# Kernel optimization log

Measured on AMD Instinct MI355X. Metric: run time of the kernel, lower is better.

## Reference

```python
import jax, jax.numpy as jnp
import numpy as np

B, N, D, H = 32, 128, 64, 128


def setup_inputs() -> dict:
    key = jax.random.key(0)
    ks = jax.random.split(key, 16)
    s = 0.05
    inp = {
        "x": jax.random.normal(ks[0], (B, N, D), dtype=jnp.float32),
        "masks": jax.random.randint(ks[1], (B, N), 0, 2, dtype=jnp.int32),
        # message_net: Linear(2D,H) -> ReLU -> Linear(H,H)
        "W1": jax.random.normal(ks[2], (2 * D, H), dtype=jnp.float32) * s,
        "b1": jax.random.normal(ks[3], (H,), dtype=jnp.float32) * s,
        "W2": jax.random.normal(ks[4], (H, H), dtype=jnp.float32) * s,
        "b2": jax.random.normal(ks[5], (H,), dtype=jnp.float32) * s,
        # attention_net: Linear(2D,H) -> ReLU -> Linear(H,1)
        "A1": jax.random.normal(ks[6], (2 * D, H), dtype=jnp.float32) * s,
        "ab1": jax.random.normal(ks[7], (H,), dtype=jnp.float32) * s,
        "A2": jax.random.normal(ks[8], (H, 1), dtype=jnp.float32) * s,
        "ab2": jax.random.normal(ks[9], (1,), dtype=jnp.float32) * s,
        # update_net: Linear(D+H,H) -> ReLU -> Linear(H,D)
        "U1": jax.random.normal(ks[10], (D + H, H), dtype=jnp.float32) * s,
        "ub1": jax.random.normal(ks[11], (H,), dtype=jnp.float32) * s,
        "U2": jax.random.normal(ks[12], (H, D), dtype=jnp.float32) * s,
        "ub2": jax.random.normal(ks[13], (D,), dtype=jnp.float32) * s,
    }
    return inp


def reference(x, masks, W1, b1, W2, b2, A1, ab1, A2, ab2, U1, ub1, U2, ub2):
    d = x.shape[-1]
    # pairs = cat([x_i, x_j]); Linear(pairs) == x_i @ W[:d] + x_j @ W[d:] + b
    # message MLP hidden: (B, N, N, H)
    h = jax.nn.relu(
        jnp.einsum("bid,dh->bih", x, W1[:d])[:, :, None, :]
        + jnp.einsum("bjd,dh->bjh", x, W1[d:])[:, None, :, :]
        + b1
    )
    messages = jnp.einsum("bijh,hk->bijk", h, W2) + b2  # (B, N, N, H)
    # attention MLP
    ha = jax.nn.relu(
        jnp.einsum("bid,dh->bih", x, A1[:d])[:, :, None, :]
        + jnp.einsum("bjd,dh->bjh", x, A1[d:])[:, None, :, :]
        + ab1
    )
    logits = jnp.einsum("bijh,h->bij", ha, A2[:, 0]) + ab2[0]  # (B, N, N)
    m = masks.astype(bool)[:, None, :]  # mask over j (source agents)
    logits = jnp.where(m, logits, -jnp.inf)
    attn = jax.nn.softmax(logits, axis=-1)
    attn = jnp.where(m, attn, 0.0)
    agg = jnp.einsum("bijh,bij->bih", messages, attn)  # (B, N, H)
    comb = jnp.concatenate([x, agg], axis=-1)  # (B, N, D+H)
    upd = jax.nn.relu(comb @ U1 + ub1) @ U2 + ub2  # (B, N, D)
    return x + upd
```

## Files before the change

kernel.cpp:

```cpp
#include <hip/hip_runtime.h>
#include <hip/hip_bf16.h>
#include <stdint.h>

#define NN 128
#define DD 64
#define HH 128

__device__ __forceinline__ float bflo(uint32_t u){ union{uint32_t u;float f;} c; c.u = u<<16; return c.f; }
__device__ __forceinline__ float bfhi(uint32_t u){ union{uint32_t u;float f;} c; c.u = u & 0xffff0000u; return c.f; }
__device__ __forceinline__ uint32_t packbf(float lo, float hi){
  __hip_bfloat16 a = __float2bfloat16(lo);
  __hip_bfloat16 b = __float2bfloat16(hi);
  uint16_t ua = *(uint16_t*)&a, ub = *(uint16_t*)&b;
  return (uint32_t)ua | ((uint32_t)ub<<16);
}

__global__ __launch_bounds__(128) void k1_proj(
    const float* __restrict__ x,
    const float* __restrict__ W1, const float* __restrict__ b1,
    const float* __restrict__ A1, const float* __restrict__ ab1,
    const float* __restrict__ W2, const float* __restrict__ b2,
    const float* __restrict__ U1, const float* __restrict__ ub1,
    float* __restrict__ Pm, float* __restrict__ Pa,
    uint32_t* __restrict__ Qmp, uint32_t* __restrict__ Qap,
    float* __restrict__ M, float* __restrict__ c0){
  const int bid = blockIdx.x;
  const int t = threadIdx.x;
  if(bid >= 512){
    int hb = bid - 512;
    if(hb < HH){
      float acc = 0.f;
      #pragma unroll 4
      for(int k=0;k<HH;k++) acc += W2[hb*HH+k] * U1[(DD+k)*HH+t];
      M[hb*HH+t] = acc;
    } else {
      float acc = ub1[t];
      #pragma unroll 4
      for(int k=0;k<HH;k++) acc += b2[k] * U1[(DD+k)*HH+t];
      c0[t] = acc;
    }
    return;
  }
  const int g = bid & 15, b = bid >> 4;
  const int jb = g*4;
  __shared__ float xs[8][64];
  __shared__ float qmS[8][128];
  __shared__ float qaS[8][128];
  {
    int r = t >> 4, d4 = (t & 15)*4;
    int gr = (r<4) ? (jb+r) : (jb + r - 4 + 64);
    *(float4*)&xs[r][d4] = *(const float4*)&x[(b*NN+gr)*DD + d4];
  }
  __syncthreads();
  float pm[8], qm[8], pa[8], qa[8];
  #pragma unroll
  for(int r=0;r<8;r++){ pm[r]=0.f;qm[r]=0.f;pa[r]=0.f;qa[r]=0.f; }
  for(int d0=0; d0<DD; d0+=4){
    float4 xr[8];
    #pragma unroll
    for(int r=0;r<8;r++) xr[r] = *(const float4*)&xs[r][d0];
    #pragma unroll
    for(int dd=0; dd<4; dd++){
      const int d = d0 + dd;
      float w1a = W1[d*HH + t];
      float w1b = W1[(DD+d)*HH + t];
      float a1a = A1[d*HH + t];
      float a1b = A1[(DD+d)*HH + t];
      #pragma unroll
      for(int r=0;r<8;r++){
        float xv = (&xr[r].x)[dd];
        pm[r] += xv*w1a; qm[r] += xv*w1b;
        pa[r] += xv*a1a; qa[r] += xv*a1b;
      }
    }
  }
  float b1v = b1[t], ab1v = ab1[t];
  #pragma unroll
  for(int r=0;r<8;r++){
    int gr = (r<4) ? (jb+r) : (jb + r - 4 + 64);
    Pm[(b*NN+gr)*HH + t] = pm[r] + b1v;
    Pa[(b*NN+gr)*HH + t] = pa[r] + ab1v;
    qmS[r][t] = qm[r];
    qaS[r][t] = qa[r];
  }
  __syncthreads();
  #pragma unroll
  for(int k=0;k<4;k++){
    int idx = t + k*128;
    int r = idx >> 6, hp = idx & 63;
    int gr = (r<4) ? (jb+r) : (jb + r - 4 + 64);
    Qmp[(b*NN+gr)*64 + hp] = packbf(qmS[r][hp], qmS[r][hp+64]);
    Qap[(b*NN+gr)*64 + hp] = packbf(qaS[r][hp], qaS[r][hp+64]);
  }
}

__global__ __launch_bounds__(256) void k2_attn_hbar(
    const float* __restrict__ Pa, const float* __restrict__ Pm,
    const uint32_t* __restrict__ Qap, const uint32_t* __restrict__ Qmp,
    const float* __restrict__ A2, const int* __restrict__ masks,
    float* __restrict__ hbar){
  const int it = blockIdx.x;
  const int b  = blockIdx.y;
  const int t = threadIdx.x;
  const int wave = t>>6, lane = t&63;
  __shared__ uint32_t qbuf[NN*65];
  __shared__ float pS[8*HH];
  __shared__ float a2S[HH];
  __shared__ float atS[8*NN];
  {
    const uint32_t* src = Qap + (size_t)b*NN*64;
    #pragma unroll
    for(int k=0;k<8;k++){
      int idx4 = t + k*256;
      int j = idx4 >> 4, hp4 = (idx4 & 15)*4;
      uint4 v = *(const uint4*)&src[j*64 + hp4];
      uint32_t* d = &qbuf[j*65 + hp4];
      d[0]=v.x; d[1]=v.y; d[2]=v.z; d[3]=v.w;
    }
    int r = t>>5, h4 = (t&31)*4;
    *(float4*)&pS[r*HH + h4] = *(const float4*)&Pa[(b*NN + it*8 + r)*HH + h4];
    if(t < HH) a2S[t] = A2[t];
  }
  __syncthreads();
  const int i0 = wave*2, i1 = i0+1;
  float a00=0.f,a01=0.f,a10=0.f,a11=0.f;
  for(int h0=0; h0<64; h0+=4){
    float4 p0a = *(const float4*)&pS[i0*HH + h0];
    float4 p0b = *(const float4*)&pS[i0*HH + 64 + h0];
    float4 p1a = *(const float4*)&pS[i1*HH + h0];
    float4 p1b = *(const float4*)&pS[i1*HH + 64 + h0];
    float4 a2a = *(const float4*)&a2S[h0];
    float4 a2b = *(const float4*)&a2S[64 + h0];
    #pragma unroll
    for(int dd=0; dd<4; dd++){
      uint32_t q0 = qbuf[lane*65 + h0 + dd];
      uint32_t q1 = qbuf[(lane+64)*65 + h0 + dd];
      float q0l=bflo(q0), q0h=bfhi(q0), q1l=bflo(q1), q1h=bfhi(q1);
      float pa0=(&p0a.x)[dd], pb0=(&p0b.x)[dd];
      float pa1=(&p1a.x)[dd], pb1=(&p1b.x)[dd];
      float aa=(&a2a.x)[dd],  ab=(&a2b.x)[dd];
      a00 += fmaxf(pa0+q0l,0.f)*aa; a00 += fmaxf(pb0+q0h,0.f)*ab;
      a01 += fmaxf(pa0+q1l,0.f)*aa; a01 += fmaxf(pb0+q1h,0.f)*ab;
      a10 += fmaxf(pa1+q0l,0.f)*aa; a10 += fmaxf(pb1+q0h,0.f)*ab;
      a11 += fmaxf(pa1+q1l,0.f)*aa; a11 += fmaxf(pb1+q1h,0.f)*ab;
    }
  }
  const int m0 = masks[b*NN + lane];
  const int m1 = masks[b*NN + 64 + lane];
  const float NEG = -3.0e38f;
  #pragma unroll
  for(int ii=0; ii<2; ii++){
    float x0 = ii ? a10 : a00, x1 = ii ? a11 : a01;
    int il = ii ? i1 : i0;
    float l0 = m0 ? x0 : NEG, l1 = m1 ? x1 : NEG;
    float v = fmaxf(l0, l1);
    for(int off=32; off>=1; off>>=1) v = fmaxf(v, __shfl_xor(v, off));
    float e0 = m0 ? __expf(x0 - v) : 0.f;
    float e1 = m1 ? __expf(x1 - v) : 0.f;
    float s = e0 + e1;
    for(int off=32; off>=1; off>>=1) s += __shfl_xor(s, off);
    float inv = (s > 0.f) ? (1.f/s) : 0.f;
    atS[il*NN + lane]      = e0*inv;
    atS[il*NN + 64 + lane] = e1*inv;
  }
  __syncthreads();
  {
    const uint32_t* src = Qmp + (size_t)b*NN*64;
    #pragma unroll
    for(int k=0;k<8;k++){
      int idx4 = t + k*256;
      int j = idx4 >> 4, hp4 = (idx4 & 15)*4;
      uint4 v = *(const uint4*)&src[j*64 + hp4];
      uint32_t* d = &qbuf[j*65 + hp4];
      d[0]=v.x; d[1]=v.y; d[2]=v.z; d[3]=v.w;
    }
    int r = t>>5, h4 = (t&31)*4;
    *(float4*)&pS[r*HH + h4] = *(const float4*)&Pm[(b*NN + it*8 + r)*HH + h4];
  }
  __syncthreads();
  float pm00 = pS[i0*HH + lane], pm01 = pS[i0*HH + 64 + lane];
  float pm10 = pS[i1*HH + lane], pm11 = pS[i1*HH + 64 + lane];
  float h00=0.f,h01=0.f,h10=0.f,h11=0.f;
  for(int j0=0; j0<NN; j0+=4){
    float4 at0 = *(const float4*)&atS[i0*NN + j0];
    float4 at1 = *(const float4*)&atS[i1*NN + j0];
    #pragma unroll
    for(int dd=0; dd<4; dd++){
      uint32_t qd = qbuf[(j0+dd)*65 + lane];
      float ql = bflo(qd), qh = bfhi(qd);
      float w0 = (&at0.x)[dd], w1 = (&at1.x)[dd];
      h00 += w0*fmaxf(pm00+ql,0.f);
      h01 += w0*fmaxf(pm01+qh,0.f);
      h10 += w1*fmaxf(pm10+ql,0.f);
      h11 += w1*fmaxf(pm11+qh,0.f);
    }
  }
  const int gi0 = b*NN + it*8 + i0, gi1 = gi0 + 1;
  hbar[gi0*HH + lane]      = h00;
  hbar[gi0*HH + 64 + lane] = h01;
  hbar[gi1*HH + lane]      = h10;
  hbar[gi1*HH + 64 + lane] = h11;
}

__global__ __launch_bounds__(256) void k3_update(
    const float* __restrict__ x, const float* __restrict__ hbar,
    const float* __restrict__ M, const float* __restrict__ c0,
    const float* __restrict__ U1, const float* __restrict__ U2,
    const float* __restrict__ ub2, float* __restrict__ out){
  const int bid = blockIdx.x;
  const int t = threadIdx.x;
  const int r0 = bid*16;
  __shared__ float xs[16][64];
  __shared__ float hb[16][128];
  __shared__ float hidS[16][128];
  __shared__ float c0S[128];
  {
    int r = t>>4, d4 = (t&15)*4;
    *(float4*)&xs[r][d4] = *(const float4*)&x[(r0+r)*DD + d4];
    int r1 = t>>5, h4 = (t&31)*4;
    *(float4*)&hb[r1][h4]   = *(const float4*)&hbar[(r0+r1)*HH + h4];
    *(float4*)&hb[r1+8][h4] = *(const float4*)&hbar[(r0+r1+8)*HH + h4];
    if(t<128) c0S[t] = c0[t];
  }
  __syncthreads();
  {
    const int c = t & 127, g = t>>7;
    float acc[8];
    #pragma unroll
    for(int r=0;r<8;r++) acc[r]=0.f;
    for(int d0=0; d0<DD; d0+=4){
      float4 xr[8];
      #pragma unroll
      for(int r=0;r<8;r++) xr[r] = *(const float4*)&xs[g*8+r][d0];
      #pragma unroll
      for(int dd=0; dd<4; dd++){
        float u = U1[(d0+dd)*HH + c];
        #pragma unroll
        for(int r=0;r<8;r++) acc[r] += (&xr[r].x)[dd]*u;
      }
    }
    for(int h0=0; h0<HH; h0+=4){
      float4 hr[8];
      #pragma unroll
      for(int r=0;r<8;r++) hr[r] = *(const float4*)&hb[g*8+r][h0];
      #pragma unroll
      for(int dd=0; dd<4; dd++){
        float mv = M[(h0+dd)*HH + c];
        #pragma unroll
        for(int r=0;r<8;r++) acc[r] += (&hr[r].x)[dd]*mv;
      }
    }
    float cc = c0S[c];
    #pragma unroll
    for(int r=0;r<8;r++) hidS[g*8+r][c] = fmaxf(acc[r]+cc, 0.f);
  }
  __syncthreads();
  {
    const int dcol = t & 63, rg = t>>6;
    float acc2[4];
    #pragma unroll
    for(int r=0;r<4;r++) acc2[r]=0.f;
    for(int ci=0; ci<HH; ci+=4){
      float4 hr[4];
      #pragma unroll
      for(int r=0;r<4;r++) hr[r] = *(const float4*)&hidS[rg*4+r][ci];
      #pragma unroll
      for(int dd=0; dd<4; dd++){
        float u2 = U2[(ci+dd)*DD + dcol];
        #pragma unroll
        for(int r=0;r<4;r++) acc2[r] += (&hr[r].x)[dd]*u2;
      }
    }
    float ub = ub2[dcol];
    #pragma unroll
    for(int r=0;r<4;r++){
      int row = r0 + rg*4 + r;
      out[row*DD + dcol] = xs[rg*4+r][dcol] + acc2[r] + ub;
    }
  }
}

extern "C" void kernel_launch(void* const* d_in, const int* in_sizes, int n_in,
                              void* d_out, int out_size, void* d_ws, size_t ws_size,
                              hipStream_t stream){
  const float* x   = (const float*)d_in[0];
  const int*   msk = (const int*)d_in[1];
  const float* W1  = (const float*)d_in[2];
  const float* b1  = (const float*)d_in[3];
  const float* W2  = (const float*)d_in[4];
  const float* b2  = (const float*)d_in[5];
  const float* A1  = (const float*)d_in[6];
  const float* ab1 = (const float*)d_in[7];
  const float* A2  = (const float*)d_in[8];
  const float* U1  = (const float*)d_in[10];
  const float* ub1 = (const float*)d_in[11];
  const float* U2  = (const float*)d_in[12];
  const float* ub2 = (const float*)d_in[13];
  float* out = (float*)d_out;

  char* w = (char*)d_ws;
  float*    Pm   = (float*)(w);
  float*    Pa   = (float*)(w + (2u<<20));
  uint32_t* Qmp  = (uint32_t*)(w + (4u<<20));
  uint32_t* Qap  = (uint32_t*)(w + (5u<<20));
  float*    hbar = (float*)(w + (6u<<20));
  float*    M    = (float*)(w + (8u<<20));
  float*    c0   = (float*)(w + (8u<<20) + (64u<<10));

  hipLaunchKernelGGL(k1_proj, dim3(641), dim3(128), 0, stream,
                     x, W1, b1, A1, ab1, W2, b2, U1, ub1,
                     Pm, Pa, Qmp, Qap, M, c0);
  hipLaunchKernelGGL(k2_attn_hbar, dim3(16,32), dim3(256), 0, stream,
                     Pa, Pm, Qap, Qmp, A2, msk, hbar);
  hipLaunchKernelGGL(k3_update, dim3(256), dim3(256), 0, stream,
                     x, hbar, M, c0, U1, U2, ub2, out);
}
```

Before: 125.0 us.

## Fuse update MLP into attention kernel and vectorize LDS access

Merges the update MLP (k3) into the attention/aggregation kernel, so hbar stays in shared memory and one launch plus a global round trip go away. The attention logit loop now reads the bf16 Q buffer with 16-byte vector loads, using a padded stride of 68 and an interleaved layout for P and A2. The update matmuls use float4 reads of U1 and M per thread. In exchange, each 8-row block redoes the U1/M/U2 weight reads, and shared memory use per block grows, which may lower occupancy.

```diff
diff --git a/kernel.cpp b/kernel.cpp
--- a/kernel.cpp
+++ b/kernel.cpp
@@ -5,6 +5,7 @@
 #define NN 128
 #define DD 64
 #define HH 128
+#define QPAD 68
 
 __device__ __forceinline__ float bflo(uint32_t u){ union{uint32_t u;float f;} c; c.u = u<<16; return c.f; }
 __device__ __forceinline__ float bfhi(uint32_t u){ union{uint32_t u;float f;} c; c.u = u & 0xffff0000u; return c.f; }
@@ -13,6 +14,17 @@
   __hip_bfloat16 b = __float2bfloat16(hi);
   uint16_t ua = *(uint16_t*)&a, ub = *(uint16_t*)&b;
   return (uint32_t)ua | ((uint32_t)ub<<16);
+}
+
+__device__ __forceinline__ void acc4(uint32_t qd0, uint32_t qd1,
+                                     float2 p0, float2 p1, float2 a2,
+                                     float2& A00, float2& A01, float2& A10, float2& A11){
+  float2 q0 = make_float2(bflo(qd0), bfhi(qd0));
+  float2 q1 = make_float2(bflo(qd1), bfhi(qd1));
+  A00.x += fmaxf(p0.x+q0.x,0.f)*a2.x; A00.y += fmaxf(p0.y+q0.y,0.f)*a2.y;
+  A01.x += fmaxf(p0.x+q1.x,0.f)*a2.x; A01.y += fmaxf(p0.y+q1.y,0.f)*a2.y;
+  A10.x += fmaxf(p1.x+q0.x,0.f)*a2.x; A10.y += fmaxf(p1.y+q0.y,0.f)*a2.y;
+  A11.x += fmaxf(p1.x+q1.x,0.f)*a2.x; A11.y += fmaxf(p1.y+q1.y,0.f)*a2.y;
 }
 
 __global__ __launch_bounds__(128) void k1_proj(
@@ -94,74 +106,86 @@
   }
 }
 
-__global__ __launch_bounds__(256) void k2_attn_hbar(
+__global__ __launch_bounds__(256) void k2_fused(
     const float* __restrict__ Pa, const float* __restrict__ Pm,
     const uint32_t* __restrict__ Qap, const uint32_t* __restrict__ Qmp,
     const float* __restrict__ A2, const int* __restrict__ masks,
-    float* __restrict__ hbar){
+    const float* __restrict__ M, const float* __restrict__ c0,
+    const float* __restrict__ U1, const float* __restrict__ U2,
+    const float* __restrict__ ub2, const float* __restrict__ x,
+    float* __restrict__ out){
   const int it = blockIdx.x;
   const int b  = blockIdx.y;
   const int t = threadIdx.x;
   const int wave = t>>6, lane = t&63;
-  __shared__ uint32_t qbuf[NN*65];
-  __shared__ float pS[8*HH];
-  __shared__ float a2S[HH];
+  __shared__ uint32_t qbuf[NN*QPAD];
+  __shared__ float pSi[8*HH];
+  __shared__ float a2i[HH];
   __shared__ float atS[8*NN];
+  __shared__ float hbS[8*HH];
+  __shared__ float hidS[8*HH];
+  __shared__ float xs[8][64];
+  __shared__ float c0S[HH];
+  const int i0 = wave*2, i1 = i0+1;
+  const int row0 = b*NN + it*8;
   {
     const uint32_t* src = Qap + (size_t)b*NN*64;
     #pragma unroll
     for(int k=0;k<8;k++){
       int idx4 = t + k*256;
       int j = idx4 >> 4, hp4 = (idx4 & 15)*4;
-      uint4 v = *(const uint4*)&src[j*64 + hp4];
-      uint32_t* d = &qbuf[j*65 + hp4];
-      d[0]=v.x; d[1]=v.y; d[2]=v.z; d[3]=v.w;
-    }
-    int r = t>>5, h4 = (t&31)*4;
-    *(float4*)&pS[r*HH + h4] = *(const float4*)&Pa[(b*NN + it*8 + r)*HH + h4];
-    if(t < HH) a2S[t] = A2[t];
-  }
-  __syncthreads();
-  const int i0 = wave*2, i1 = i0+1;
-  float a00=0.f,a01=0.f,a10=0.f,a11=0.f;
-  for(int h0=0; h0<64; h0+=4){
-    float4 p0a = *(const float4*)&pS[i0*HH + h0];
-    float4 p0b = *(const float4*)&pS[i0*HH + 64 + h0];
-    float4 p1a = *(const float4*)&pS[i1*HH + h0];
-    float4 p1b = *(const float4*)&pS[i1*HH + 64 + h0];
-    float4 a2a = *(const float4*)&a2S[h0];
-    float4 a2b = *(const float4*)&a2S[64 + h0];
-    #pragma unroll
-    for(int dd=0; dd<4; dd++){
-      uint32_t q0 = qbuf[lane*65 + h0 + dd];
-      uint32_t q1 = qbuf[(lane+64)*65 + h0 + dd];
-      float q0l=bflo(q0), q0h=bfhi(q0), q1l=bflo(q1), q1h=bfhi(q1);
-      float pa0=(&p0a.x)[dd], pb0=(&p0b.x)[dd];
-      float pa1=(&p1a.x)[dd], pb1=(&p1b.x)[dd];
-      float aa=(&a2a.x)[dd],  ab=(&a2b.x)[dd];
-      a00 += fmaxf(pa0+q0l,0.f)*aa; a00 += fmaxf(pb0+q0h,0.f)*ab;
-      a01 += fmaxf(pa0+q1l,0.f)*aa; a01 += fmaxf(pb0+q1h,0.f)*ab;
-      a10 += fmaxf(pa1+q0l,0.f)*aa; a10 += fmaxf(pb1+q0h,0.f)*ab;
-      a11 += fmaxf(pa1+q1l,0.f)*aa; a11 += fmaxf(pb1+q1h,0.f)*ab;
-    }
+      *(uint4*)&qbuf[j*QPAD + hp4] = *(const uint4*)&src[j*64 + hp4];
+    }
+    #pragma unroll
+    for(int k=0;k<4;k++){
+      int idx = t + k*256;
+      int r = idx>>7, rem = idx&127, h2 = rem&63, half = rem>>6;
+      pSi[r*HH + 2*h2 + half] = Pa[(row0 + r)*HH + h2 + 64*half];
+    }
+    if(t < HH) a2i[2*(t&63) + (t>>6)] = A2[t];
+    if(t < 128){ int r = t>>4, d4 = (t&15)*4;
+      *(float4*)&xs[r][d4] = *(const float4*)&x[(row0 + r)*DD + d4]; }
+    else { int u = t-128; if(u < HH) c0S[u] = c0[u]; }
   }
   const int m0 = masks[b*NN + lane];
   const int m1 = masks[b*NN + 64 + lane];
-  const float NEG = -3.0e38f;
-  #pragma unroll
-  for(int ii=0; ii<2; ii++){
-    float x0 = ii ? a10 : a00, x1 = ii ? a11 : a01;
-    int il = ii ? i1 : i0;
-    float l0 = m0 ? x0 : NEG, l1 = m1 ? x1 : NEG;
-    float v = fmaxf(l0, l1);
-    for(int off=32; off>=1; off>>=1) v = fmaxf(v, __shfl_xor(v, off));
-    float e0 = m0 ? __expf(x0 - v) : 0.f;
-    float e1 = m1 ? __expf(x1 - v) : 0.f;
-    float s = e0 + e1;
-    for(int off=32; off>=1; off>>=1) s += __shfl_xor(s, off);
-    float inv = (s > 0.f) ? (1.f/s) : 0.f;
-    atS[il*NN + lane]      = e0*inv;
-    atS[il*NN + 64 + lane] = e1*inv;
+  __syncthreads();
+  {
+    float2 A00=make_float2(0.f,0.f), A01=A00, A10=A00, A11=A00;
+    for(int hp0=0; hp0<64; hp0+=4){
+      uint4 q0 = *(const uint4*)&qbuf[lane*QPAD + hp0];
+      uint4 q1 = *(const uint4*)&qbuf[(lane+64)*QPAD + hp0];
+      float4 p0a = *(const float4*)&pSi[i0*HH + 2*hp0];
+      float4 p0b = *(const float4*)&pSi[i0*HH + 2*hp0 + 4];
+      float4 p1a = *(const float4*)&pSi[i1*HH + 2*hp0];
+      float4 p1b = *(const float4*)&pSi[i1*HH + 2*hp0 + 4];
+      float4 aa  = *(const float4*)&a2i[2*hp0];
+      float4 ab  = *(const float4*)&a2i[2*hp0 + 4];
+      acc4(q0.x, q1.x, make_float2(p0a.x,p0a.y), make_float2(p1a.x,p1a.y),
+           make_float2(aa.x,aa.y), A00,A01,A10,A11);
+      acc4(q0.y, q1.y, make_float2(p0a.z,p0a.w), make_float2(p1a.z,p1a.w),
+           make_float2(aa.z,aa.w), A00,A01,A10,A11);
+      acc4(q0.z, q1.z, make_float2(p0b.x,p0b.y), make_float2(p1b.x,p1b.y),
+           make_float2(ab.x,ab.y), A00,A01,A10,A11);
+      acc4(q0.w, q1.w, make_float2(p0b.z,p0b.w), make_float2(p1b.z,p1b.w),
+           make_float2(ab.z,ab.w), A00,A01,A10,A11);
+    }
+    float l[2][2] = {{A00.x+A00.y, A01.x+A01.y},{A10.x+A10.y, A11.x+A11.y}};
+    const float NEG = -3.0e38f;
+    #pragma unroll
+    for(int ii=0; ii<2; ii++){
+      float x0 = l[ii][0], x1 = l[ii][1];
+      int il = i0 + ii;
+      float v = fmaxf(m0 ? x0 : NEG, m1 ? x1 : NEG);
+      for(int off=32; off>=1; off>>=1) v = fmaxf(v, __shfl_xor(v, off));
+      float e0 = m0 ? __expf(x0 - v) : 0.f;
+      float e1 = m1 ? __expf(x1 - v) : 0.f;
+      float s = e0 + e1;
+      for(int off=32; off>=1; off>>=1) s += __shfl_xor(s, off);
+      float inv = (s > 0.f) ? (1.f/s) : 0.f;
+      atS[il*NN + lane]      = e0*inv;
+      atS[il*NN + 64 + lane] = e1*inv;
+    }
   }
   __syncthreads();
   {
@@ -170,113 +194,81 @@
     for(int k=0;k<8;k++){
       int idx4 = t + k*256;
       int j = idx4 >> 4, hp4 = (idx4 & 15)*4;
-      uint4 v = *(const uint4*)&src[j*64 + hp4];
-      uint32_t* d = &qbuf[j*65 + hp4];
-      d[0]=v.x; d[1]=v.y; d[2]=v.z; d[3]=v.w;
-    }
-    int r = t>>5, h4 = (t&31)*4;
-    *(float4*)&pS[r*HH + h4] = *(const float4*)&Pm[(b*NN + it*8 + r)*HH + h4];
-  }
-  __syncthreads();
-  float pm00 = pS[i0*HH + lane], pm01 = pS[i0*HH + 64 + lane];
-  float pm10 = pS[i1*HH + lane], pm11 = pS[i1*HH + 64 + lane];
-  float h00=0.f,h01=0.f,h10=0.f,h11=0.f;
-  for(int j0=0; j0<NN; j0+=4){
-    float4 at0 = *(const float4*)&atS[i0*NN + j0];
-    float4 at1 = *(const float4*)&atS[i1*NN + j0];
-    #pragma unroll
-    for(int dd=0; dd<4; dd++){
-      uint32_t qd = qbuf[(j0+dd)*65 + lane];
-      float ql = bflo(qd), qh = bfhi(qd);
-      float w0 = (&at0.x)[dd], w1 = (&at1.x)[dd];
-      h00 += w0*fmaxf(pm00+ql,0.f);
-      h01 += w0*fmaxf(pm01+qh,0.f);
-      h10 += w1*fmaxf(pm10+ql,0.f);
-      h11 += w1*fmaxf(pm11+qh,0.f);
-    }
-  }
-  const int gi0 = b*NN + it*8 + i0, gi1 = gi0 + 1;
-  hbar[gi0*HH + lane]      = h00;
-  hbar[gi0*HH + 64 + lane] = h01;
-  hbar[gi1*HH + lane]      = h10;
-  hbar[gi1*HH + 64 + lane] = h11;
-}
-
-__global__ __launch_bounds__(256) void k3_update(
-    const float* __restrict__ x, const float* __restrict__ hbar,
-    const float* __restrict__ M, const float* __restrict__ c0,
-    const float* __restrict__ U1, const float* __restrict__ U2,
-    const float* __restrict__ ub2, float* __restrict__ out){
-  const int bid = blockIdx.x;
-  const int t = threadIdx.x;
-  const int r0 = bid*16;
-  __shared__ float xs[16][64];
-  __shared__ float hb[16][128];
-  __shared__ float hidS[16][128];
-  __shared__ float c0S[128];
-  {
-    int r = t>>4, d4 = (t&15)*4;
-    *(float4*)&xs[r][d4] = *(const float4*)&x[(r0+r)*DD + d4];
-    int r1 = t>>5, h4 = (t&31)*4;
-    *(float4*)&hb[r1][h4]   = *(const float4*)&hbar[(r0+r1)*HH + h4];
-    *(float4*)&hb[r1+8][h4] = *(const float4*)&hbar[(r0+r1+8)*HH + h4];
-    if(t<128) c0S[t] = c0[t];
-  }
-  __syncthreads();
-  {
-    const int c = t & 127, g = t>>7;
-    float acc[8];
-    #pragma unroll
-    for(int r=0;r<8;r++) acc[r]=0.f;
+      *(uint4*)&qbuf[j*QPAD + hp4] = *(const uint4*)&src[j*64 + hp4];
+    }
+    #pragma unroll
+    for(int k=0;k<4;k++){
+      int idx = t + k*256;
+      int r = idx>>7, rem = idx&127, h2 = rem&63, half = rem>>6;
+      pSi[r*HH + 2*h2 + half] = Pm[(row0 + r)*HH + h2 + 64*half];
+    }
+  }
+  __syncthreads();
+  {
+    float2 pm0 = *(const float2*)&pSi[i0*HH + 2*lane];
+    float2 pm1 = *(const float2*)&pSi[i1*HH + 2*lane];
+    float2 H0 = make_float2(0.f,0.f), H1 = H0;
+    for(int j0=0; j0<NN; j0+=4){
+      float4 at0 = *(const float4*)&atS[i0*NN + j0];
+      float4 at1 = *(const float4*)&atS[i1*NN + j0];
+      #pragma unroll
+      for(int dd=0; dd<4; dd++){
+        uint32_t qd = qbuf[(j0+dd)*QPAD + lane];
+        float ql = bflo(qd), qh = bfhi(qd);
+        float w0 = (&at0.x)[dd], w1 = (&at1.x)[dd];
+        H0.x += w0*fmaxf(pm0.x+ql,0.f); H0.y += w0*fmaxf(pm0.y+qh,0.f);
+        H1.x += w1*fmaxf(pm1.x+ql,0.f); H1.y += w1*fmaxf(pm1.y+qh,0.f);
+      }
+    }
+    hbS[i0*HH + lane]      = H0.x;
+    hbS[i0*HH + 64 + lane] = H0.y;
+    hbS[i1*HH + lane]      = H1.x;
+    hbS[i1*HH + 64 + lane] = H1.y;
+  }
+  __syncthreads();
+  {
+    const int r = t>>5, c4 = (t&31)*4;
+    float4 acc = *(const float4*)&c0S[c4];
     for(int d0=0; d0<DD; d0+=4){
-      float4 xr[8];
-      #pragma unroll
-      for(int r=0;r<8;r++) xr[r] = *(const float4*)&xs[g*8+r][d0];
+      float4 xv4 = *(const float4*)&xs[r][d0];
       #pragma unroll
       for(int dd=0; dd<4; dd++){
-        float u = U1[(d0+dd)*HH + c];
-        #pragma unroll
-        for(int r=0;r<8;r++) acc[r] += (&xr[r].x)[dd]*u;
+        float4 u = *(const float4*)&U1[(d0+dd)*HH + c4];
+        float xv = (&xv4.x)[dd];
+        acc.x += xv*u.x; acc.y += xv*u.y; acc.z += xv*u.z; acc.w += xv*u.w;
       }
     }
     for(int h0=0; h0<HH; h0+=4){
-      float4 hr[8];
-      #pragma unroll
-      for(int r=0;r<8;r++) hr[r] = *(const float4*)&hb[g*8+r][h0];
+      float4 hv4 = *(const float4*)&hbS[r*HH + h0];
       #pragma unroll
       for(int dd=0; dd<4; dd++){
-        float mv = M[(h0+dd)*HH + c];
-        #pragma unroll
-        for(int r=0;r<8;r++) acc[r] += (&hr[r].x)[dd]*mv;
-      }
-    }
-    float cc = c0S[c];
-    #pragma unroll
-    for(int r=0;r<8;r++) hidS[g*8+r][c] = fmaxf(acc[r]+cc, 0.f);
-  }
-  __syncthreads();
-  {
-    const int dcol = t & 63, rg = t>>6;
-    float acc2[4];
-    #pragma unroll
-    for(int r=0;r<4;r++) acc2[r]=0.f;
+        float4 m = *(const float4*)&M[(h0+dd)*HH + c4];
+        float hv = (&hv4.x)[dd];
+        acc.x += hv*m.x; acc.y += hv*m.y; acc.z += hv*m.z; acc.w += hv*m.w;
+      }
+    }
+    float4 hid;
+    hid.x = fmaxf(acc.x,0.f); hid.y = fmaxf(acc.y,0.f);
+    hid.z = fmaxf(acc.z,0.f); hid.w = fmaxf(acc.w,0.f);
+    *(float4*)&hidS[r*HH + c4] = hid;
+  }
+  __syncthreads();
+  {
+    const int r = t>>5, dc2 = (t&31)*2;
+    float2 acc2 = make_float2(0.f,0.f);
     for(int ci=0; ci<HH; ci+=4){
-      float4 hr[4];
-      #pragma unroll
-      for(int r=0;r<4;r++) hr[r] = *(const float4*)&hidS[rg*4+r][ci];
+      float4 hv4 = *(const float4*)&hidS[r*HH + ci];
       #pragma unroll
       for(int dd=0; dd<4; dd++){
-        float u2 = U2[(ci+dd)*DD + dcol];
-        #pragma unroll
-        for(int r=0;r<4;r++) acc2[r] += (&hr[r].x)[dd]*u2;
-      }
-    }
-    float ub = ub2[dcol];
-    #pragma unroll
-    for(int r=0;r<4;r++){
-      int row = r0 + rg*4 + r;
-      out[row*DD + dcol] = xs[rg*4+r][dcol] + acc2[r] + ub;
-    }
+        float2 u2 = *(const float2*)&U2[(ci+dd)*DD + dc2];
+        float hv = (&hv4.x)[dd];
+        acc2.x += hv*u2.x; acc2.y += hv*u2.y;
+      }
+    }
+    float2 ub = *(const float2*)&ub2[dc2];
+    float2 xv = *(const float2*)&xs[r][dc2];
+    float2 o = make_float2(xv.x + acc2.x + ub.x, xv.y + acc2.y + ub.y);
+    *(float2*)&out[(row0 + r)*DD + dc2] = o;
   }
 }
 
@@ -303,15 +295,12 @@
   float*    Pa   = (float*)(w + (2u<<20));
   uint32_t* Qmp  = (uint32_t*)(w + (4u<<20));
   uint32_t* Qap  = (uint32_t*)(w + (5u<<20));
-  float*    hbar = (float*)(w + (6u<<20));
-  float*    M    = (float*)(w + (8u<<20));
-  float*    c0   = (float*)(w + (8u<<20) + (64u<<10));
+  float*    M    = (float*)(w + (6u<<20));
+  float*    c0   = (float*)(w + (6u<<20) + (64u<<10));
 
   hipLaunchKernelGGL(k1_proj, dim3(641), dim3(128), 0, stream,
                      x, W1, b1, A1, ab1, W2, b2, U1, ub1,
                      Pm, Pa, Qmp, Qap, M, c0);
-  hipLaunchKernelGGL(k2_attn_hbar, dim3(16,32), dim3(256), 0, stream,
-                     Pa, Pm, Qap, Qmp, A2, msk, hbar);
-  hipLaunchKernelGGL(k3_update, dim3(256), dim3(256), 0, stream,
-                     x, hbar, M, c0, U1, U2, ub2, out);
-}
+  hipLaunchKernelGGL(k2_fused, dim3(16,32), dim3(256), 0, stream,
+                     Pa, Pm, Qap, Qmp, A2, msk, M, c0, U1, U2, ub2, x, out);
+}
```

Measured after the change: 126.3 us. Within noise of the previous version (+1.0%).
